# Kernel optimization log

Measured on AMD Instinct MI355X. Metric: run time of the kernel, lower is better.

Reference implementation:

```python
import jax, jax.numpy as jnp
import numpy as np

SOS = 1  # vocab.word2idx[SYM_SOS]


def _lstm_cell(x, h, c, Wih, Whh, b):
    # PyTorch LSTMCell gate order: i, f, g, o
    g = x @ Wih.T + h @ Whh.T + b
    i, f, gg, o = jnp.split(g, 4, axis=-1)
    c2 = jax.nn.sigmoid(f) * c + jax.nn.sigmoid(i) * jnp.tanh(gg)
    h2 = jax.nn.sigmoid(o) * jnp.tanh(c2)
    return h2, c2


def _attention(q, m, Wq, Wm, b, v):
    # additive attention: q [B,Dq], m [B,N,Dm] -> context [B,Dm]
    e = jnp.tanh((q @ Wq)[:, None, :] + m @ Wm + b)      # [B,N,H]
    score = jnp.einsum('bnh,h->bn', e, v)                # [B,N]
    a = jax.nn.softmax(score, axis=-1)
    return jnp.einsum('bn,bnd->bd', a, m)


def setup_inputs() -> dict:
    key = jax.random.key(0)
    ks = iter(jax.random.split(key, 32))
    B, T, V = 128, 20, 20000
    DI, DW, H = 512, 512, 1024
    s = 0.02
    d = {}
    d['img_feats'] = jax.random.normal(next(ks), (B, 36, DI), jnp.float32)
    d['ppl_feats'] = jax.random.normal(next(ks), (B, 100, DI), jnp.float32)
    d['answer_hint'] = jax.random.normal(next(ks), (B, DW), jnp.float32)
    d['question'] = jax.random.randint(next(ks), (B, T), 0, V)
    d['emb'] = jax.random.normal(next(ks), (V, DW), jnp.float32) * s
    d['pool_Wq'] = jax.random.normal(next(ks), (DW, DW), jnp.float32) * s
    d['pool_Wm'] = jax.random.normal(next(ks), (DI, DW), jnp.float32) * s
    d['pool_b'] = jnp.zeros((DW,), jnp.float32)
    d['pool_v'] = jax.random.normal(next(ks), (DW,), jnp.float32) * s
    d['img_Wq'] = jax.random.normal(next(ks), (H, H), jnp.float32) * s
    d['img_Wm'] = jax.random.normal(next(ks), (DI, H), jnp.float32) * s
    d['img_b'] = jnp.zeros((H,), jnp.float32)
    d['img_v'] = jax.random.normal(next(ks), (H,), jnp.float32) * s
    d['ppl_Wq'] = jax.random.normal(next(ks), (H, H), jnp.float32) * s
    d['ppl_Wm'] = jax.random.normal(next(ks), (DI, H), jnp.float32) * s
    d['ppl_b'] = jnp.zeros((H,), jnp.float32)
    d['ppl_v'] = jax.random.normal(next(ks), (H,), jnp.float32) * s
    d['vis_Wih'] = jax.random.normal(next(ks), (4 * H, DI + DW), jnp.float32) * s
    d['vis_Whh'] = jax.random.normal(next(ks), (4 * H, H), jnp.float32) * s
    d['vis_b'] = jnp.zeros((4 * H,), jnp.float32)
    d['lang_Wih'] = jax.random.normal(next(ks), (4 * H, H + DI), jnp.float32) * s
    d['lang_Whh'] = jax.random.normal(next(ks), (4 * H, H), jnp.float32) * s
    d['lang_b'] = jnp.zeros((4 * H,), jnp.float32)
    d['proj_W'] = jax.random.normal(next(ks), (H, V), jnp.float32) * s
    d['proj_b'] = jnp.zeros((V,), jnp.float32)
    return d


def reference(img_feats, ppl_feats, answer_hint, question, emb,
              pool_Wq, pool_Wm, pool_b, pool_v,
              img_Wq, img_Wm, img_b, img_v,
              ppl_Wq, ppl_Wm, ppl_b, ppl_v,
              vis_Wih, vis_Whh, vis_b,
              lang_Wih, lang_Whh, lang_b,
              proj_W, proj_b):
    B, T = question.shape
    H = vis_Whh.shape[1]
    # pooled image feature from answer hint (computed once)
    img_pool = _attention(answer_hint, img_feats, pool_Wq, pool_Wm, pool_b, pool_v)
    # teacher forcing inputs: SOS then question[:, :-1]
    tokens_in = jnp.concatenate(
        [jnp.full((B, 1), SOS, question.dtype), question[:, :-1]], axis=1)

    def step(carry, tok):
        h_vis, c_vis, h_lang, c_lang = carry
        dec_emb = jax.nn.relu(emb[tok])                          # [B,DW]
        x_vis = jnp.concatenate([img_pool, dec_emb], axis=-1)
        h_vis, c_vis = _lstm_cell(x_vis, h_vis, c_vis, vis_Wih, vis_Whh, vis_b)
        image_attn = _attention(h_vis, img_feats, img_Wq, img_Wm, img_b, img_v)
        ppl_attn = _attention(h_vis, ppl_feats, ppl_Wq, ppl_Wm, ppl_b, ppl_v)
        x_lang = jnp.concatenate([image_attn + ppl_attn, h_vis], axis=-1)
        h_lang, c_lang = _lstm_cell(x_lang, h_lang, c_lang, lang_Wih, lang_Whh, lang_b)
        logp = jax.nn.log_softmax(h_lang @ proj_W + proj_b, axis=-1)
        return (h_vis, c_vis, h_lang, c_lang), (logp, jnp.argmax(logp, axis=-1))

    z = jnp.zeros((B, H), img_feats.dtype)
    _, (logps, toks) = jax.lax.scan(step, (z, z, z, z), tokens_in.T)
    return jnp.transpose(logps, (1, 0, 2)), toks.T


if __name__ == '__main__':
    out = reference(**setup_inputs())
    print(out[0].shape, out[1].shape)
```

## Files before the change

kernel.cpp:

```cpp
#include <hip/hip_runtime.h>
#include <cstddef>
#include <cstdint>

using u16 = unsigned short;
typedef float    f32x4 __attribute__((ext_vector_type(4)));
typedef _Float16 f16x8 __attribute__((ext_vector_type(8)));
typedef u16      us8   __attribute__((ext_vector_type(8)));

constexpr int B  = 128;
constexpr int T  = 20;
constexpr int V  = 20000;
constexpr int DW = 512;
constexpr int H  = 1024;
constexpr int G4 = 4096;
constexpr int NI = 36;
constexpr int NP = 100;
constexpr int SOS = 1;

__device__ __forceinline__ float sigf(float x) { return 1.0f / (1.0f + expf(-x)); }
__device__ __forceinline__ u16 f16bits(_Float16 h) { u16 u; __builtin_memcpy(&u, &h, 2); return u; }
__device__ __forceinline__ float h2f(u16 u) { _Float16 h; __builtin_memcpy(&h, &u, 2); return (float)h; }

template<bool WSIDE>
__device__ __forceinline__ void split1(float x, u16& b0, u16& b1, u16& b2) {
    _Float16 h  = (_Float16)x;
    float    hf = (float)h;
    _Float16 lo = (_Float16)((x - hf) * 64.0f);
    _Float16 hs = (_Float16)(hf * (1.0f / 64.0f));
    b0 = f16bits(h);
    if constexpr (WSIDE) { b1 = f16bits(hs); b2 = f16bits(lo); }
    else                 { b1 = f16bits(lo); b2 = f16bits(hs); }
}

template<int BM, int BN, bool HAS_ADD, bool HAS_BIAS, int NSW = 0, bool OUTF16 = false>
__global__ __launch_bounds__(256)
void gemm3(const u16* __restrict__ A, const u16* __restrict__ Bt,
           const float* __restrict__ Add, const float* __restrict__ bias,
           void* __restrict__ Cv, int N, int K3)
{
    __shared__ __align__(16) u16 As[BM * 64];
    __shared__ __align__(16) u16 Bs[BN * 64];
    constexpr int FR = BM / 32, FC = BN / 32, PA = BM / 32, PB = BN / 32;
    const int tid  = threadIdx.x;
    int bx = blockIdx.x, by = blockIdx.y;
    if constexpr (NSW > 0) {
        const int nt = (int)gridDim.x, mt = (int)gridDim.y;
        const int lin = by * nt + bx;
        const int sc0 = (lin / (NSW * mt)) * NSW;
        const int w   = (NSW < nt - sc0) ? NSW : (nt - sc0);
        const int r   = lin - sc0 * mt;
        bx = sc0 + r % w;
        by = r / w;
    }
    const int bm   = by * BM, bn = bx * BN;
    const int lane = tid & 63, wid = tid >> 6;
    const int wm   = (wid >> 1) * (BM / 2), wn = (wid & 1) * (BN / 2);
    const int srow = tid >> 3;
    const int scol = (tid & 7) * 8;

    f32x4 acc[FR][FC] = {};
    us8 ra[PA], rb[PB];

    auto ldg = [&](int k0) {
#pragma unroll
        for (int p = 0; p < PA; ++p)
            ra[p] = *(const us8*)(A + (size_t)(bm + p * 32 + srow) * K3 + k0 + scol);
#pragma unroll
        for (int p = 0; p < PB; ++p) {
            int n = bn + p * 32 + srow; if (n > N - 1) n = N - 1;
            rb[p] = *(const us8*)(Bt + (size_t)n * K3 + k0 + scol);
        }
    };
    ldg(0);

    for (int k0 = 0; k0 < K3; k0 += 64) {
        __syncthreads();
#pragma unroll
        for (int p = 0; p < PA; ++p) {
            const int row = p * 32 + srow;
            *(us8*)((char*)As + row * 128 + ((scol * 2) ^ ((row & 7) << 4))) = ra[p];
        }
#pragma unroll
        for (int p = 0; p < PB; ++p) {
            const int row = p * 32 + srow;
            *(us8*)((char*)Bs + row * 128 + ((scol * 2) ^ ((row & 7) << 4))) = rb[p];
        }
        __syncthreads();
        if (k0 + 64 < K3) ldg(k0 + 64);
#pragma unroll
        for (int ks = 0; ks < 2; ++ks) {
            f16x8 af[FR], bf[FC];
#pragma unroll
            for (int m = 0; m < FR; ++m) {
                const int row = wm + m * 16 + (lane & 15);
                const int cb  = (ks * 64 + ((lane >> 4) << 4)) ^ ((row & 7) << 4);
                af[m] = *(const f16x8*)((const char*)As + row * 128 + cb);
            }
#pragma unroll
            for (int n = 0; n < FC; ++n) {
                const int row = wn + n * 16 + (lane & 15);
                const int cb  = (ks * 64 + ((lane >> 4) << 4)) ^ ((row & 7) << 4);
                bf[n] = *(const f16x8*)((const char*)Bs + row * 128 + cb);
            }
#pragma unroll
            for (int m = 0; m < FR; ++m)
#pragma unroll
                for (int n = 0; n < FC; ++n)
                    acc[m][n] = __builtin_amdgcn_mfma_f32_16x16x32_f16(af[m], bf[n], acc[m][n], 0, 0, 0);
        }
    }
#pragma unroll
    for (int m = 0; m < FR; ++m) {
        const int r0 = bm + wm + m * 16 + ((lane >> 4) << 2);
#pragma unroll
        for (int n = 0; n < FC; ++n) {
            const int c = bn + wn + n * 16 + (lane & 15);
            if (c < N) {
#pragma unroll
                for (int j = 0; j < 4; ++j) {
                    float v = acc[m][n][j];
                    if constexpr (HAS_ADD)  v += Add[(size_t)(r0 + j) * N + c];
                    if constexpr (HAS_BIAS) v += bias[c];
                    if constexpr (OUTF16)
                        ((u16*)Cv)[(size_t)(r0 + j) * N + c] = f16bits((_Float16)v);
                    else
                        ((float*)Cv)[(size_t)(r0 + j) * N + c] = v;
                }
            }
        }
    }
}

template<int EPI, int BN, int BK>
__device__ __forceinline__ void gemm_core(
    u16* __restrict__ As, u16* __restrict__ Bs,
    const u16* __restrict__ A, const u16* __restrict__ Bt,
    const float* __restrict__ Add, const float* __restrict__ bias,
    float* __restrict__ CS, u16* __restrict__ o1, u16* __restrict__ o2,
    int N, int K3, int t, int bx, int by)
{
    constexpr int NA8  = BK / 32;
    constexpr int TPRB = 256 / BN;
    constexpr int NB8  = (BK / TPRB) / 8;
    constexpr int NFC  = BN / 16;
    const int tid  = threadIdx.x;
    const int bn   = bx * BN, bm = by * 64;
    const int lane = tid & 63, wv = tid >> 6;
    const int rowA = tid >> 2;
    const int scA  = (tid & 3) * (BK / 4);
    const int rowB = tid / TPRB;
    const int scB  = (tid % TPRB) * (BK / TPRB);
    const int swzA = (rowA & 7) << 4;
    const int swzB = (rowB & 7) << 4;
    const u16* Ap = A  + (size_t)(bm + rowA) * K3 + scA;
    const u16* Bp = Bt + (size_t)(bn + rowB) * K3 + scB;
    char* Awp = (char*)As + rowA * (BK * 2);
    char* Bwp = (char*)Bs + rowB * (BK * 2);
    const int arow = wv * 16 + (lane & 15);
    const char* Arp = (const char*)As + arow * (BK * 2);
    const int aswz = (arow & 7) << 4;
    const int jl   = lane & 15;

    f32x4 acc[NFC] = {};
    us8 ra[NA8], rb[NB8];
#pragma unroll
    for (int i = 0; i < NA8; ++i) ra[i] = *(const us8*)(Ap + 8 * i);
#pragma unroll
    for (int i = 0; i < NB8; ++i) rb[i] = *(const us8*)(Bp + 8 * i);

    for (int k0 = 0; k0 < K3; k0 += BK) {
        __syncthreads();
#pragma unroll
        for (int i = 0; i < NA8; ++i)
            *(us8*)(Awp + ((scA * 2 + 16 * i) ^ swzA)) = ra[i];
#pragma unroll
        for (int i = 0; i < NB8; ++i)
            *(us8*)(Bwp + ((scB * 2 + 16 * i) ^ swzB)) = rb[i];
        __syncthreads();
        if (k0 + BK < K3) {
#pragma unroll
            for (int i = 0; i < NA8; ++i) ra[i] = *(const us8*)(Ap + k0 + BK + 8 * i);
#pragma unroll
            for (int i = 0; i < NB8; ++i) rb[i] = *(const us8*)(Bp + k0 + BK + 8 * i);
        }
#pragma unroll
        for (int ks = 0; ks < BK / 32; ++ks) {
            const int cb = ks * 64 + ((lane >> 4) << 4);
            const f16x8 af = *(const f16x8*)(Arp + (cb ^ aswz));
#pragma unroll
            for (int g = 0; g < NFC; ++g) {
                const int brow = g * 16 + jl;
                const f16x8 bf = *(const f16x8*)((const char*)Bs + brow * (BK * 2) + (cb ^ ((brow & 7) << 4)));
                acc[g] = __builtin_amdgcn_mfma_f32_16x16x32_f16(af, bf, acc[g], 0, 0, 0);
            }
        }
    }
    const int rb0 = bm + wv * 16 + ((lane >> 4) << 2);
    if constexpr (EPI == 0) {
#pragma unroll
        for (int g = 0; g < NFC; ++g) {
            const int c = bn + g * 16 + jl;
#pragma unroll
            for (int jj = 0; jj < 4; ++jj)
                CS[(size_t)(rb0 + jj) * N + c] = acc[g][jj];
        }
    } else {
        const int j = bx * 16 + jl;
#pragma unroll
        for (int jj = 0; jj < 4; ++jj) {
            const int b = rb0 + jj;
            float gi = acc[0][jj], gf = acc[1][jj], gg = acc[2][jj], go = acc[3][jj];
            if constexpr (EPI == 1) {
                const float* ap = Add + (size_t)b * 4096 + bn + jl;
                gi += ap[0]; gf += ap[16]; gg += ap[32]; go += ap[48];
            } else {
                const float* bp = bias + bn + jl;
                gi += bp[0]; gf += bp[16]; gg += bp[32]; go += bp[48];
            }
            const float c = sigf(gf) * CS[b * 1024 + j] + sigf(gi) * tanhf(gg);
            const float h = sigf(go) * tanhf(c);
            CS[b * 1024 + j] = c;
            u16 b0, b1, b2; split1<false>(h, b0, b1, b2);
            if constexpr (EPI == 1) {
                u16* a = o1 + (size_t)b * 3072 + j;
                a[0] = b0; a[1024] = b1; a[2048] = b2;
                u16* x = o2 + (size_t)b * 7680 + 512 + j;
                x[0] = b0; x[2560] = b1; x[5120] = b2;
            } else {
                u16* x = o1 + (size_t)b * 7680 + 1536 + j;
                x[0] = b0; x[2560] = b1; x[5120] = b2;
                u16* hh = o2 + ((size_t)b * T + t) * 3072 + j;
                hh[0] = b0; hh[1024] = b1; hh[2048] = b2;
            }
        }
    }
}

__global__ __launch_bounds__(256)
void gemm_q(const u16* __restrict__ A, const u16* __restrict__ Bt,
            float* __restrict__ CS, int N, int K3)
{
    __shared__ __align__(16) u16 As[64 * 384];
    __shared__ __align__(16) u16 Bs[32 * 384];
    gemm_core<0, 32, 384>(As, Bs, A, Bt, nullptr, nullptr, CS, nullptr, nullptr,
                          N, K3, 0, blockIdx.x, blockIdx.y);
}

__global__ __launch_bounds__(256)
void step_combo(const u16* __restrict__ lang_A, const u16* __restrict__ langW3,
                const float* __restrict__ lang_bi, float* __restrict__ c_lang,
                u16* __restrict__ lang_o1, u16* __restrict__ h3_all,
                const u16* __restrict__ vis_A, const u16* __restrict__ visWhh3,
                const float* __restrict__ g_pre_t, float* __restrict__ c_vis,
                u16* __restrict__ vis_o1, u16* __restrict__ vis_o2, int t)
{
    __shared__ __align__(16) u16 As[64 * 384];
    __shared__ __align__(16) u16 Bs[64 * 384];
    if (blockIdx.z == 0) {
        if (t >= 1)
            gemm_core<2, 64, 384>(As, Bs, lang_A, langW3, nullptr, lang_bi,
                                  c_lang, lang_o1, h3_all, G4, 7680, t - 1,
                                  blockIdx.x, blockIdx.y);
    } else {
        if (t < T)
            gemm_core<1, 64, 384>(As, Bs, vis_A, visWhh3, g_pre_t, nullptr,
                                  c_vis, vis_o1, vis_o2, G4, 3072, t,
                                  blockIdx.x, blockIdx.y);
    }
}

template<bool WSIDE>
__global__ __launch_bounds__(256)
void split3_rows(const float* __restrict__ src, int ld, int K8,
                 u16* __restrict__ out, int Kt, int coloff)
{
    const int idx = blockIdx.x * 256 + threadIdx.x;
    const int r = idx / K8, kk = (idx - r * K8) * 8;
    const float* s = src + (size_t)r * ld + kk;
    const float4 x0 = *(const float4*)s, x1 = *(const float4*)(s + 4);
    float xs[8] = {x0.x, x0.y, x0.z, x0.w, x1.x, x1.y, x1.z, x1.w};
    us8 h, m, l;
#pragma unroll
    for (int j = 0; j < 8; ++j) { u16 a, b, c; split1<WSIDE>(xs[j], a, b, c); h[j]=a; m[j]=b; l[j]=c; }
    u16* o = out + (size_t)r * (3 * Kt) + coloff + kk;
    *(us8*)o = h; *(us8*)(o + Kt) = m; *(us8*)(o + 2 * Kt) = l;
}

__global__ __launch_bounds__(256)
void split3_lstm(const float* __restrict__ src, int ld, int K8,
                 u16* __restrict__ out, int Kt, int coloff)
{
    const int idx = blockIdx.x * 256 + threadIdx.x;
    const int r = idx / K8, kk = (idx - r * K8) * 8;
    const int g = r >> 10, j = r & 1023;
    const int orow = ((j >> 4) << 6) + (g << 4) + (j & 15);
    const float* s = src + (size_t)r * ld + kk;
    const float4 x0 = *(const float4*)s, x1 = *(const float4*)(s + 4);
    float xs[8] = {x0.x, x0.y, x0.z, x0.w, x1.x, x1.y, x1.z, x1.w};
    us8 h, m, l;
#pragma unroll
    for (int jj = 0; jj < 8; ++jj) { u16 a, b, c; split1<true>(xs[jj], a, b, c); h[jj]=a; m[jj]=b; l[jj]=c; }
    u16* o = out + (size_t)orow * (3 * Kt) + coloff + kk;
    *(us8*)o = h; *(us8*)(o + Kt) = m; *(us8*)(o + 2 * Kt) = l;
}

__global__ __launch_bounds__(256)
void permute_bias_lstm(const float* __restrict__ b, float* __restrict__ out)
{
    const int c = blockIdx.x * 256 + threadIdx.x;
    const int jg = c >> 6, g = (c >> 4) & 3, jlo = c & 15;
    out[c] = b[g * 1024 + jg * 16 + jlo];
}

__global__ __launch_bounds__(256)
void transpose_split3_w(const float* __restrict__ W, int N, int K,
                        u16* __restrict__ out)
{
    const int n0 = blockIdx.x * 64, k0 = blockIdx.y * 64;
    const int tid = threadIdx.x;
    __shared__ float ts[64][65];
    for (int i = 0; i < 16; ++i) {
        const int idx = i * 256 + tid;
        const int kl = idx >> 6, nl = idx & 63;
        float v = 0.f;
        if (n0 + nl < N) v = W[(size_t)(k0 + kl) * N + n0 + nl];
        ts[nl][kl] = v;
    }
    __syncthreads();
    for (int i = 0; i < 2; ++i) {
        const int idx = i * 256 + tid;
        const int nl = idx >> 3, kc = (idx & 7) * 8;
        if (n0 + nl < N) {
            us8 h, m, l;
#pragma unroll
            for (int j = 0; j < 8; ++j) {
                u16 a, b, c; split1<true>(ts[nl][kc + j], a, b, c);
                h[j] = a; m[j] = b; l[j] = c;
            }
            u16* o = out + (size_t)(n0 + nl) * (3 * K) + k0 + kc;
            *(us8*)o = h; *(us8*)(o + K) = m; *(us8*)(o + 2 * K) = l;
        }
    }
}

__global__ __launch_bounds__(256)
void embed_relu3(const int* __restrict__ question, const float* __restrict__ emb,
                 u16* __restrict__ demb3)
{
    const int idx = blockIdx.x * 256 + threadIdx.x;
    const int r = idx >> 6, kk = (idx & 63) * 8;
    const int t = r / B, b = r - t * B;
    const int tok = (t == 0) ? SOS : question[b * T + t - 1];
    const float* s = emb + (size_t)tok * DW + kk;
    const float4 x0 = *(const float4*)s, x1 = *(const float4*)(s + 4);
    float xs[8] = {x0.x, x0.y, x0.z, x0.w, x1.x, x1.y, x1.z, x1.w};
    us8 h, m, l;
#pragma unroll
    for (int j = 0; j < 8; ++j) {
        u16 a, b2, c; split1<false>(fmaxf(xs[j], 0.f), a, b2, c);
        h[j] = a; m[j] = b2; l[j] = c;
    }
    u16* o = demb3 + (size_t)r * 1536 + kk;
    *(us8*)o = h; *(us8*)(o + 512) = m; *(us8*)(o + 1024) = l;
}

__global__ __launch_bounds__(256)
void attn_score(const float* __restrict__ q, int qld,
                const float* __restrict__ mW, const float* __restrict__ v,
                float* __restrict__ score, int Nn, int Hd)
{
    const int n = blockIdx.x, b = blockIdx.y;
    const float* qp = q + (size_t)b * qld;
    const float* mp = mW + ((size_t)b * Nn + n) * Hd;
    float s = 0.f;
    for (int h = threadIdx.x; h < Hd; h += 256)
        s += tanhf(qp[h] + mp[h]) * v[h];
    __shared__ float red[4];
    const int lane = threadIdx.x & 63, wv = threadIdx.x >> 6;
    for (int o = 32; o; o >>= 1) s += __shfl_down(s, o, 64);
    if (lane == 0) red[wv] = s;
    __syncthreads();
    if (threadIdx.x == 0) score[(size_t)b * Nn + n] = red[0] + red[1] + red[2] + red[3];
}

__global__ __launch_bounds__(256)
void attn_ctx_pool(const float* __restrict__ score, const float* __restrict__ m,
                   u16* __restrict__ out3, int Nn)
{
    constexpr int D = 512;
    const int b = blockIdx.x;
    __shared__ float aw[128];
    __shared__ float red[8];
    const int tid = threadIdx.x, lane = tid & 63, wv = tid >> 6;
    float mx = -3.4e38f;
    for (int n = tid; n < Nn; n += 256) mx = fmaxf(mx, score[(size_t)b * Nn + n]);
    for (int o = 32; o; o >>= 1) mx = fmaxf(mx, __shfl_down(mx, o, 64));
    if (lane == 0) red[wv] = mx;
    __syncthreads();
    mx = fmaxf(fmaxf(red[0], red[1]), fmaxf(red[2], red[3]));
    float se = 0.f;
    for (int n = tid; n < Nn; n += 256) {
        float e = expf(score[(size_t)b * Nn + n] - mx);
        aw[n] = e; se += e;
    }
    for (int o = 32; o; o >>= 1) se += __shfl_down(se, o, 64);
    if (lane == 0) red[4 + wv] = se;
    __syncthreads();
    const float inv = 1.0f / (red[4] + red[5] + red[6] + red[7]);
    for (int d = tid; d < D; d += 256) {
        float s = 0.f;
        for (int n = 0; n < Nn; ++n) s += aw[n] * m[((size_t)b * Nn + n) * D + d];
        s *= inv;
        u16 b0, b1, b2; split1<false>(s, b0, b1, b2);
        u16* o = out3 + (size_t)b * 1536 + d;
        o[0] = b0; o[512] = b1; o[1024] = b2;
    }
}

__global__ __launch_bounds__(512)
void attn_fused(const float* __restrict__ qbuf,
                const u16* __restrict__ img_mW, const u16* __restrict__ ppl_mW,
                const float* __restrict__ img_v, const float* __restrict__ ppl_v,
                const float* __restrict__ img_feats, const float* __restrict__ ppl_feats,
                u16* __restrict__ x3)
{
    const int b = blockIdx.x;
    const int tid = threadIdx.x, lane = tid & 63, wv = tid >> 6;
    __shared__ float qs[2048];
    __shared__ float vs[2048];
    __shared__ float aw[136];
    __shared__ float awn[136];

    for (int i = tid; i < 2048; i += 512) {
        qs[i] = qbuf[(size_t)b * 2048 + i];
        vs[i] = (i < 1024) ? img_v[i] : ppl_v[i - 1024];
    }
    __syncthreads();

    for (int n = wv; n < NI; n += 8) {
        const u16* mp = img_mW + ((size_t)b * NI + n) * 1024;
        float s = 0.f;
#pragma unroll
        for (int u = 0; u < 2; ++u) {
            const int h = (lane + 64 * u) * 8;
            const us8 m8 = *(const us8*)(mp + h);
#pragma unroll
            for (int j = 0; j < 8; ++j)
                s += tanhf(qs[h + j] + h2f(m8[j])) * vs[h + j];
        }
        for (int o = 1; o < 64; o <<= 1) s += __shfl_xor(s, o, 64);
        if (lane == 0) aw[n] = s;
    }
    for (int n = wv; n < NP; n += 8) {
        const u16* mp = ppl_mW + ((size_t)b * NP + n) * 1024;
        float s = 0.f;
#pragma unroll
        for (int u = 0; u < 2; ++u) {
            const int h = (lane + 64 * u) * 8;
            const us8 m8 = *(const us8*)(mp + h);
#pragma unroll
            for (int j = 0; j < 8; ++j)
                s += tanhf(qs[1024 + h + j] + h2f(m8[j])) * vs[1024 + h + j];
        }
        for (int o = 1; o < 64; o <<= 1) s += __shfl_xor(s, o, 64);
        if (lane == 0) aw[36 + n] = s;
    }
    __syncthreads();

    if (wv == 0) {
        const float x = (lane < NI) ? aw[lane] : -3.4e38f;
        float mx = x;
        for (int o = 1; o < 64; o <<= 1) mx = fmaxf(mx, __shfl_xor(mx, o, 64));
        const float e = (lane < NI) ? expf(x - mx) : 0.f;
        float ss = e;
        for (int o = 1; o < 64; o <<= 1) ss += __shfl_xor(ss, o, 64);
        if (lane < NI) awn[lane] = e / ss;
    } else if (wv == 1) {
        const float x0 = aw[36 + lane];
        const float x1 = (lane < NP - 64) ? aw[100 + lane] : -3.4e38f;
        float mx = fmaxf(x0, x1);
        for (int o = 1; o < 64; o <<= 1) mx = fmaxf(mx, __shfl_xor(mx, o, 64));
        const float e0 = expf(x0 - mx);
        const float e1 = (lane < NP - 64) ? expf(x1 - mx) : 0.f;
        float ss = e0 + e1;
        for (int o = 1; o < 64; o <<= 1) ss += __shfl_xor(ss, o, 64);
        awn[36 + lane] = e0 / ss;
        if (lane < NP - 64) awn[100 + lane] = e1 / ss;
    }
    __syncthreads();

    {
        const int d = tid;
        float s = 0.f;
        const float* ip = img_feats + (size_t)b * NI * 512 + d;
#pragma unroll 4
        for (int n = 0; n < NI; ++n) s += awn[n] * ip[n * 512];
        const float* pp = ppl_feats + (size_t)b * NP * 512 + d;
#pragma unroll 4
        for (int n = 0; n < NP; ++n) s += awn[36 + n] * pp[n * 512];
        u16 b0, b1, b2; split1<false>(s, b0, b1, b2);
        u16* o = x3 + (size_t)b * 7680 + d;
        o[0] = b0; o[2560] = b1; o[5120] = b2;
    }
}

__global__ __launch_bounds__(256)
void add_bcast(float* __restrict__ g_pre, const float* __restrict__ g_const)
{
    const int idx = blockIdx.x * 256 + threadIdx.x;
    const int bg = idx % (B * G4 / 4);
    float4 a = ((float4*)g_pre)[idx];
    const float4 c = ((const float4*)g_const)[bg];
    a.x += c.x; a.y += c.y; a.z += c.z; a.w += c.w;
    ((float4*)g_pre)[idx] = a;
}

__global__ __launch_bounds__(256)
void zero_f(float* __restrict__ p) { p[blockIdx.x * 256 + threadIdx.x] = 0.f; }

__global__ __launch_bounds__(256)
void zero_u32(unsigned int* __restrict__ p) { p[blockIdx.x * 256 + threadIdx.x] = 0u; }

__global__ __launch_bounds__(256)
void logsm_argmax(float* __restrict__ out)
{
    const int r = blockIdx.x;
    float* row = out + (size_t)r * V;
    const int tid = threadIdx.x, lane = tid & 63, wv = tid >> 6;
    float m = -3.4e38f, s = 0.f; int mi = 0;
    for (int i4 = tid; i4 < V / 4; i4 += 256) {
        const float4 x4 = ((const float4*)row)[i4];
        const float xs[4] = {x4.x, x4.y, x4.z, x4.w};
#pragma unroll
        for (int j = 0; j < 4; ++j) {
            const float x = xs[j];
            if (x > m) { s = s * expf(m - x) + 1.f; m = x; mi = i4 * 4 + j; }
            else       s += expf(x - m);
        }
    }
    for (int o = 1; o < 64; o <<= 1) {
        const float m2 = __shfl_xor(m, o, 64);
        const float s2 = __shfl_xor(s, o, 64);
        const int  mi2 = __shfl_xor(mi, o, 64);
        if (m2 > m || (m2 == m && mi2 < mi)) { s = s2 + s * expf(m - m2); m = m2; mi = mi2; }
        else s += s2 * expf(m2 - m);
    }
    __shared__ float sm[4], ssm[4]; __shared__ int smi[4];
    __shared__ float lse_sh; __shared__ int mi_sh;
    if (lane == 0) { sm[wv] = m; ssm[wv] = s; smi[wv] = mi; }
    __syncthreads();
    if (tid == 0) {
        float M = sm[0], S = ssm[0]; int MI = smi[0];
        for (int w = 1; w < 4; ++w) {
            if (sm[w] > M || (sm[w] == M && smi[w] < MI)) { S = ssm[w] + S * expf(M - sm[w]); M = sm[w]; MI = smi[w]; }
            else S += ssm[w] * expf(sm[w] - M);
        }
        lse_sh = M + logf(S); mi_sh = MI;
    }
    __syncthreads();
    const float lse = lse_sh;
    for (int i4 = tid; i4 < V / 4; i4 += 256) {
        float4 x4 = ((const float4*)row)[i4];
        x4.x -= lse; x4.y -= lse; x4.z -= lse; x4.w -= lse;
        ((float4*)row)[i4] = x4;
    }
    if (tid == 0) out[(size_t)B * T * V + r] = (float)mi_sh;
}

extern "C" void kernel_launch(void* const* d_in, const int* in_sizes, int n_in,
                              void* d_out, int out_size, void* d_ws, size_t ws_size,
                              hipStream_t stream)
{
    (void)in_sizes; (void)n_in; (void)out_size; (void)ws_size;

    const float* img_feats   = (const float*)d_in[0];
    const float* ppl_feats   = (const float*)d_in[1];
    const float* answer_hint = (const float*)d_in[2];
    const int*   question    = (const int*)d_in[3];
    const float* emb         = (const float*)d_in[4];
    const float* pool_Wq     = (const float*)d_in[5];
    const float* pool_Wm     = (const float*)d_in[6];
    const float* pool_b      = (const float*)d_in[7];
    const float* pool_v      = (const float*)d_in[8];
    const float* img_Wq      = (const float*)d_in[9];
    const float* img_Wm      = (const float*)d_in[10];
    const float* img_b       = (const float*)d_in[11];
    const float* img_v       = (const float*)d_in[12];
    const float* ppl_Wq      = (const float*)d_in[13];
    const float* ppl_Wm      = (const float*)d_in[14];
    const float* ppl_b       = (const float*)d_in[15];
    const float* ppl_v       = (const float*)d_in[16];
    const float* vis_Wih     = (const float*)d_in[17];
    const float* vis_Whh     = (const float*)d_in[18];
    const float* vis_b       = (const float*)d_in[19];
    const float* lang_Wih    = (const float*)d_in[20];
    const float* lang_Whh    = (const float*)d_in[21];
    const float* lang_b      = (const float*)d_in[22];
    const float* proj_W      = (const float*)d_in[23];
    const float* proj_b      = (const float*)d_in[24];

    float* out = (float*)d_out;
    float* ws  = (float*)d_ws;

    size_t off = 0;
    auto alloc = [&](size_t nf) { size_t r = off; off += (nf + 63) & ~(size_t)63; return r; };
    const size_t regionX = off;
    float* g_pre   = ws + alloc((size_t)T * B * G4);
    float* pool_mW = ws + alloc((size_t)B * NI * DW);
    u16*   demb3   = (u16*)(ws + alloc((size_t)T * B * 1536 / 2));
    u16*   hint3   = (u16*)(ws + alloc((size_t)B * 1536 / 2));
    u16*   poolWq3t= (u16*)(ws + alloc((size_t)512 * 1536 / 2));
    u16*   poolWm3t= (u16*)(ws + alloc((size_t)512 * 1536 / 2));
    u16*   visdemb3= (u16*)(ws + alloc((size_t)G4 * 1536 / 2));
    u16*   vispool3= (u16*)(ws + alloc((size_t)G4 * 1536 / 2));
    u16* img_mW    = (u16*)(ws + alloc((size_t)B * NI * H / 2));
    u16* ppl_mW    = (u16*)(ws + alloc((size_t)B * NP * H / 2));
    u16* img3      = (u16*)(ws + alloc((size_t)B * NI * 1536 / 2));
    u16* ppl3      = (u16*)(ws + alloc((size_t)B * NP * 1536 / 2));
    u16* imgpool3  = (u16*)(ws + alloc((size_t)B * 1536 / 2));
    u16* visWhh3   = (u16*)(ws + alloc((size_t)G4 * 3072 / 2));
    u16* langW3    = (u16*)(ws + alloc((size_t)G4 * 7680 / 2));
    u16* wq3t      = (u16*)(ws + alloc((size_t)2048 * 3072 / 2));
    u16* imgWm3t   = (u16*)(ws + alloc((size_t)1024 * 1536 / 2));
    u16* pplWm3t   = (u16*)(ws + alloc((size_t)1024 * 1536 / 2));
    float* c_vis   = ws + alloc((size_t)B * H);
    float* c_lang  = ws + alloc((size_t)B * H);
    u16* a3        = (u16*)(ws + alloc((size_t)2 * B * 3072 / 2));
    u16* x3        = (u16*)(ws + alloc((size_t)2 * B * 7680 / 2));
    u16* h3_all    = (u16*)(ws + alloc((size_t)B * T * 3072 / 2));
    float* qbuf    = ws + alloc((size_t)B * 2048);
    float* g_const = ws + alloc((size_t)B * G4);
    float* vis_bi  = ws + alloc((size_t)G4);
    float* lang_bi = ws + alloc((size_t)G4);
    float* pool_qW = ws + alloc((size_t)B * DW);
    float* pool_sc = ws + alloc((size_t)B * NI);
    u16* projW3t   = (u16*)(ws + regionX);

    const dim3 blk(256);

    zero_f<<<dim3((2 * B * H) / 256), blk, 0, stream>>>(c_vis);
    zero_u32<<<dim3((2 * B * 3072 + 2 * B * 7680) / 2 / 256), blk, 0, stream>>>((unsigned int*)a3);

    embed_relu3<<<dim3(T * B * 64 / 256), blk, 0, stream>>>(question, emb, demb3);
    permute_bias_lstm<<<dim3(16), blk, 0, stream>>>(vis_b, vis_bi);
    permute_bias_lstm<<<dim3(16), blk, 0, stream>>>(lang_b, lang_bi);
    split3_lstm<<<dim3(G4 * 64 / 256), blk, 0, stream>>>(vis_Wih + 512, 1024, 64, visdemb3, 512, 0);
    split3_lstm<<<dim3(G4 * 64 / 256), blk, 0, stream>>>(vis_Wih, 1024, 64, vispool3, 512, 0);
    split3_lstm<<<dim3(G4 * 128 / 256), blk, 0, stream>>>(vis_Whh, 1024, 128, visWhh3, 1024, 0);
    split3_lstm<<<dim3(G4 * 192 / 256), blk, 0, stream>>>(lang_Wih, 1536, 192, langW3, 2560, 0);
    split3_lstm<<<dim3(G4 * 128 / 256), blk, 0, stream>>>(lang_Whh, 1024, 128, langW3, 2560, 1536);
    split3_rows<false><<<dim3(B * NI * 64 / 256), blk, 0, stream>>>(img_feats, 512, 64, img3, 512, 0);
    split3_rows<false><<<dim3(B * NP * 64 / 256), blk, 0, stream>>>(ppl_feats, 512, 64, ppl3, 512, 0);
    split3_rows<false><<<dim3(B * 64 / 256), blk, 0, stream>>>(answer_hint, 512, 64, hint3, 512, 0);
    transpose_split3_w<<<dim3(8, 8), blk, 0, stream>>>(pool_Wq, 512, 512, poolWq3t);
    transpose_split3_w<<<dim3(8, 8), blk, 0, stream>>>(pool_Wm, 512, 512, poolWm3t);
    transpose_split3_w<<<dim3(16, 8), blk, 0, stream>>>(img_Wm, 1024, 512, imgWm3t);
    transpose_split3_w<<<dim3(16, 8), blk, 0, stream>>>(ppl_Wm, 1024, 512, pplWm3t);
    transpose_split3_w<<<dim3(16, 16), blk, 0, stream>>>(img_Wq, 1024, 1024, wq3t);
    transpose_split3_w<<<dim3(16, 16), blk, 0, stream>>>(ppl_Wq, 1024, 1024, wq3t + (size_t)1024 * 3072);

    gemm3<128, 128, false, true><<<dim3(32, 20), blk, 0, stream>>>(demb3, visdemb3, nullptr, vis_bi, g_pre, G4, 1536);
    gemm3<64, 64, false, false><<<dim3(8, 2), blk, 0, stream>>>(hint3, poolWq3t, nullptr, nullptr, pool_qW, 512, 1536);
    gemm3<128, 128, false, true><<<dim3(4, 36), blk, 0, stream>>>(img3, poolWm3t, nullptr, pool_b, pool_mW, 512, 1536);
    attn_score<<<dim3(NI, B), blk, 0, stream>>>(pool_qW, 512, pool_mW, pool_v, pool_sc, NI, 512);
    attn_ctx_pool<<<dim3(B), blk, 0, stream>>>(pool_sc, img_feats, imgpool3, NI);
    gemm3<64, 64, false, false><<<dim3(64, 2), blk, 0, stream>>>(imgpool3, vispool3, nullptr, nullptr, g_const, G4, 1536);
    add_bcast<<<dim3(T * B * G4 / 4 / 256), blk, 0, stream>>>(g_pre, g_const);
    gemm3<128, 128, false, true, 0, true><<<dim3(8, 36), blk, 0, stream>>>(img3, imgWm3t, nullptr, img_b, img_mW, H, 1536);
    gemm3<128, 128, false, true, 0, true><<<dim3(8, 100), blk, 0, stream>>>(ppl3, pplWm3t, nullptr, ppl_b, ppl_mW, H, 1536);

    for (int t = 0; t <= T; ++t) {
        u16* lang_A  = x3 + (size_t)((t + 1) & 1) * B * 7680;
        u16* lang_o1 = x3 + (size_t)(t & 1) * B * 7680;
        u16* vis_A   = a3 + (size_t)(t & 1) * B * 3072;
        u16* vis_o1  = a3 + (size_t)((t + 1) & 1) * B * 3072;
        u16* vis_o2  = x3 + (size_t)(t & 1) * B * 7680;
        const float* gp = g_pre + (size_t)(t < T ? t : 0) * B * G4;
        step_combo<<<dim3(64, 2, 2), blk, 0, stream>>>(
            lang_A, langW3, lang_bi, c_lang, lang_o1, h3_all,
            vis_A, visWhh3, gp, c_vis, vis_o1, vis_o2, t);
        if (t < T) {
            gemm_q<<<dim3(64, 2), blk, 0, stream>>>(vis_o1, wq3t, qbuf, 2048, 3072);
            attn_fused<<<dim3(B), dim3(512), 0, stream>>>(qbuf, img_mW, ppl_mW, img_v, ppl_v,
                                                          img_feats, ppl_feats, vis_o2);
        }
    }

    transpose_split3_w<<<dim3(313, 16), blk, 0, stream>>>(proj_W, V, 1024, projW3t);
    gemm3<128, 128, false, true, 20><<<dim3(157, 20), blk, 0, stream>>>(
        h3_all, projW3t, nullptr, proj_b, out, V, 3072);
    logsm_argmax<<<dim3(B * T), blk, 0, stream>>>(out);
}
```

Baseline: 3.658 ms.

## Fuse vis input GEMMs into one K=1024 GEMM and halve gemm_q tile width

The embedding and the pooled-image feature are now written side by side into one concatenated activation buffer, replicated across all T steps. A single GEMM against the full split vis_Wih then produces the precomputed gates directly. This removes the separate pooled GEMM, the broadcast-add kernel and one weight split, at the cost of a larger GEMM over the duplicated pooled rows. Separately, gemm_q uses BN=16 with twice as many blocks to fill more CUs per step, and __restrict__ is dropped from several pointer arguments.

```diff
diff --git a/kernel.cpp b/kernel.cpp
--- a/kernel.cpp
+++ b/kernel.cpp
@@ -133,10 +133,10 @@
 
 template<int EPI, int BN, int BK>
 __device__ __forceinline__ void gemm_core(
-    u16* __restrict__ As, u16* __restrict__ Bs,
-    const u16* __restrict__ A, const u16* __restrict__ Bt,
-    const float* __restrict__ Add, const float* __restrict__ bias,
-    float* __restrict__ CS, u16* __restrict__ o1, u16* __restrict__ o2,
+    u16* As, u16* Bs,
+    const u16* A, const u16* Bt,
+    const float* Add, const float* bias,
+    float* CS, u16* o1, u16* o2,
     int N, int K3, int t, int bx, int by)
 {
     constexpr int NA8  = BK / 32;
@@ -241,18 +241,18 @@
             float* __restrict__ CS, int N, int K3)
 {
     __shared__ __align__(16) u16 As[64 * 384];
-    __shared__ __align__(16) u16 Bs[32 * 384];
-    gemm_core<0, 32, 384>(As, Bs, A, Bt, nullptr, nullptr, CS, nullptr, nullptr,
+    __shared__ __align__(16) u16 Bs[16 * 384];
+    gemm_core<0, 16, 384>(As, Bs, A, Bt, nullptr, nullptr, CS, nullptr, nullptr,
                           N, K3, 0, blockIdx.x, blockIdx.y);
 }
 
 __global__ __launch_bounds__(256)
 void step_combo(const u16* __restrict__ lang_A, const u16* __restrict__ langW3,
-                const float* __restrict__ lang_bi, float* __restrict__ c_lang,
-                u16* __restrict__ lang_o1, u16* __restrict__ h3_all,
+                const float* __restrict__ lang_bi, float* c_lang,
+                u16* lang_o1, u16* h3_all,
                 const u16* __restrict__ vis_A, const u16* __restrict__ visWhh3,
-                const float* __restrict__ g_pre_t, float* __restrict__ c_vis,
-                u16* __restrict__ vis_o1, u16* __restrict__ vis_o2, int t)
+                const float* __restrict__ g_pre_t, float* c_vis,
+                u16* vis_o1, u16* vis_o2, int t)
 {
     __shared__ __align__(16) u16 As[64 * 384];
     __shared__ __align__(16) u16 Bs[64 * 384];
@@ -345,7 +345,7 @@
 
 __global__ __launch_bounds__(256)
 void embed_relu3(const int* __restrict__ question, const float* __restrict__ emb,
-                 u16* __restrict__ demb3)
+                 u16* __restrict__ A2)
 {
     const int idx = blockIdx.x * 256 + threadIdx.x;
     const int r = idx >> 6, kk = (idx & 63) * 8;
@@ -360,8 +360,8 @@
         u16 a, b2, c; split1<false>(fmaxf(xs[j], 0.f), a, b2, c);
         h[j] = a; m[j] = b2; l[j] = c;
     }
-    u16* o = demb3 + (size_t)r * 1536 + kk;
-    *(us8*)o = h; *(us8*)(o + 512) = m; *(us8*)(o + 1024) = l;
+    u16* o = A2 + (size_t)r * 3072 + 512 + kk;
+    *(us8*)o = h; *(us8*)(o + 1024) = m; *(us8*)(o + 2048) = l;
 }
 
 __global__ __launch_bounds__(256)
@@ -385,7 +385,7 @@
 
 __global__ __launch_bounds__(256)
 void attn_ctx_pool(const float* __restrict__ score, const float* __restrict__ m,
-                   u16* __restrict__ out3, int Nn)
+                   u16* __restrict__ A2, int Nn)
 {
     constexpr int D = 512;
     const int b = blockIdx.x;
@@ -412,8 +412,10 @@
         for (int n = 0; n < Nn; ++n) s += aw[n] * m[((size_t)b * Nn + n) * D + d];
         s *= inv;
         u16 b0, b1, b2; split1<false>(s, b0, b1, b2);
-        u16* o = out3 + (size_t)b * 1536 + d;
-        o[0] = b0; o[512] = b1; o[1024] = b2;
+        for (int tt = 0; tt < T; ++tt) {
+            u16* o = A2 + ((size_t)tt * B + b) * 3072 + d;
+            o[0] = b0; o[1024] = b1; o[2048] = b2;
+        }
     }
 }
 
@@ -502,17 +504,6 @@
         u16* o = x3 + (size_t)b * 7680 + d;
         o[0] = b0; o[2560] = b1; o[5120] = b2;
     }
-}
-
-__global__ __launch_bounds__(256)
-void add_bcast(float* __restrict__ g_pre, const float* __restrict__ g_const)
-{
-    const int idx = blockIdx.x * 256 + threadIdx.x;
-    const int bg = idx % (B * G4 / 4);
-    float4 a = ((float4*)g_pre)[idx];
-    const float4 c = ((const float4*)g_const)[bg];
-    a.x += c.x; a.y += c.y; a.z += c.z; a.w += c.w;
-    ((float4*)g_pre)[idx] = a;
 }
 
 __global__ __launch_bounds__(256)
@@ -607,17 +598,15 @@
     const size_t regionX = off;
     float* g_pre   = ws + alloc((size_t)T * B * G4);
     float* pool_mW = ws + alloc((size_t)B * NI * DW);
-    u16*   demb3   = (u16*)(ws + alloc((size_t)T * B * 1536 / 2));
+    u16*   A2      = (u16*)(ws + alloc((size_t)T * B * 3072 / 2));
     u16*   hint3   = (u16*)(ws + alloc((size_t)B * 1536 / 2));
     u16*   poolWq3t= (u16*)(ws + alloc((size_t)512 * 1536 / 2));
     u16*   poolWm3t= (u16*)(ws + alloc((size_t)512 * 1536 / 2));
-    u16*   visdemb3= (u16*)(ws + alloc((size_t)G4 * 1536 / 2));
-    u16*   vispool3= (u16*)(ws + alloc((size_t)G4 * 1536 / 2));
-    u16* img_mW    = (u16*)(ws + alloc((size_t)B * NI * H / 2));
-    u16* ppl_mW    = (u16*)(ws + alloc((size_t)B * NP * H / 2));
-    u16* img3      = (u16*)(ws + alloc((size_t)B * NI * 1536 / 2));
-    u16* ppl3      = (u16*)(ws + alloc((size_t)B * NP * 1536 / 2));
-    u16* imgpool3  = (u16*)(ws + alloc((size_t)B * 1536 / 2));
+    u16*   visWih3 = (u16*)(ws + alloc((size_t)G4 * 3072 / 2));
+    u16*   img_mW  = (u16*)(ws + alloc((size_t)B * NI * H / 2));
+    u16*   ppl_mW  = (u16*)(ws + alloc((size_t)B * NP * H / 2));
+    u16*   img3    = (u16*)(ws + alloc((size_t)B * NI * 1536 / 2));
+    u16*   ppl3    = (u16*)(ws + alloc((size_t)B * NP * 1536 / 2));
     u16* visWhh3   = (u16*)(ws + alloc((size_t)G4 * 3072 / 2));
     u16* langW3    = (u16*)(ws + alloc((size_t)G4 * 7680 / 2));
     u16* wq3t      = (u16*)(ws + alloc((size_t)2048 * 3072 / 2));
@@ -629,7 +618,6 @@
     u16* x3        = (u16*)(ws + alloc((size_t)2 * B * 7680 / 2));
     u16* h3_all    = (u16*)(ws + alloc((size_t)B * T * 3072 / 2));
     float* qbuf    = ws + alloc((size_t)B * 2048);
-    float* g_const = ws + alloc((size_t)B * G4);
     float* vis_bi  = ws + alloc((size_t)G4);
     float* lang_bi = ws + alloc((size_t)G4);
     float* pool_qW = ws + alloc((size_t)B * DW);
@@ -641,11 +629,10 @@
     zero_f<<<dim3((2 * B * H) / 256), blk, 0, stream>>>(c_vis);
     zero_u32<<<dim3((2 * B * 3072 + 2 * B * 7680) / 2 / 256), blk, 0, stream>>>((unsigned int*)a3);
 
-    embed_relu3<<<dim3(T * B * 64 / 256), blk, 0, stream>>>(question, emb, demb3);
+    embed_relu3<<<dim3(T * B * 64 / 256), blk, 0, stream>>>(question, emb, A2);
     permute_bias_lstm<<<dim3(16), blk, 0, stream>>>(vis_b, vis_bi);
     permute_bias_lstm<<<dim3(16), blk, 0, stream>>>(lang_b, lang_bi);
-    split3_lstm<<<dim3(G4 * 64 / 256), blk, 0, stream>>>(vis_Wih + 512, 1024, 64, visdemb3, 512, 0);
-    split3_lstm<<<dim3(G4 * 64 / 256), blk, 0, stream>>>(vis_Wih, 1024, 64, vispool3, 512, 0);
+    split3_lstm<<<dim3(G4 * 128 / 256), blk, 0, stream>>>(vis_Wih, 1024, 128, visWih3, 1024, 0);
     split3_lstm<<<dim3(G4 * 128 / 256), blk, 0, stream>>>(vis_Whh, 1024, 128, visWhh3, 1024, 0);
     split3_lstm<<<dim3(G4 * 192 / 256), blk, 0, stream>>>(lang_Wih, 1536, 192, langW3, 2560, 0);
     split3_lstm<<<dim3(G4 * 128 / 256), blk, 0, stream>>>(lang_Whh, 1024, 128, langW3, 2560, 1536);
@@ -659,13 +646,11 @@
     transpose_split3_w<<<dim3(16, 16), blk, 0, stream>>>(img_Wq, 1024, 1024, wq3t);
     transpose_split3_w<<<dim3(16, 16), blk, 0, stream>>>(ppl_Wq, 1024, 1024, wq3t + (size_t)1024 * 3072);
 
-    gemm3<128, 128, false, true><<<dim3(32, 20), blk, 0, stream>>>(demb3, visdemb3, nullptr, vis_bi, g_pre, G4, 1536);
     gemm3<64, 64, false, false><<<dim3(8, 2), blk, 0, stream>>>(hint3, poolWq3t, nullptr, nullptr, pool_qW, 512, 1536);
     gemm3<128, 128, false, true><<<dim3(4, 36), blk, 0, stream>>>(img3, poolWm3t, nullptr, pool_b, pool_mW, 512, 1536);
     attn_score<<<dim3(NI, B), blk, 0, stream>>>(pool_qW, 512, pool_mW, pool_v, pool_sc, NI, 512);
-    attn_ctx_pool<<<dim3(B), blk, 0, stream>>>(pool_sc, img_feats, imgpool3, NI);
-    gemm3<64, 64, false, false><<<dim3(64, 2), blk, 0, stream>>>(imgpool3, vispool3, nullptr, nullptr, g_const, G4, 1536);
-    add_bcast<<<dim3(T * B * G4 / 4 / 256), blk, 0, stream>>>(g_pre, g_const);
+    attn_ctx_pool<<<dim3(B), blk, 0, stream>>>(pool_sc, img_feats, A2, NI);
+    gemm3<128, 128, false, true><<<dim3(32, 20), blk, 0, stream>>>(A2, visWih3, nullptr, vis_bi, g_pre, G4, 3072);
     gemm3<128, 128, false, true, 0, true><<<dim3(8, 36), blk, 0, stream>>>(img3, imgWm3t, nullptr, img_b, img_mW, H, 1536);
     gemm3<128, 128, false, true, 0, true><<<dim3(8, 100), blk, 0, stream>>>(ppl3, pplWm3t, nullptr, ppl_b, ppl_mW, H, 1536);
 
@@ -680,7 +665,7 @@
             lang_A, langW3, lang_bi, c_lang, lang_o1, h3_all,
             vis_A, visWhh3, gp, c_vis, vis_o1, vis_o2, t);
         if (t < T) {
-            gemm_q<<<dim3(64, 2), blk, 0, stream>>>(vis_o1, wq3t, qbuf, 2048, 3072);
+            gemm_q<<<dim3(128, 2), blk, 0, stream>>>(vis_o1, wq3t, qbuf, 2048, 3072);
             attn_fused<<<dim3(B), dim3(512), 0, stream>>>(qbuf, img_mW, ppl_mW, img_v, ppl_v,
                                                           img_feats, ppl_feats, vis_o2);
         }
```

After: 3.579 ms. 2.1% less time.
